# Optimization experiments

Hardware: AMD Instinct MI355X
Metric: run time of the kernel (lower is better)

Reference implementation:

```python
import jax, jax.numpy as jnp
import numpy as np
from jax import lax

GAIN = 2.0 ** (-0.5)
EPS = 1e-8


def _modconv(x, style_vec, s_w, s_b, weight):
    # x: [b, cin, h, w]; style_vec: [b, style_dim]
    # s_w: [cin, style_dim], s_b: [cin]; weight: [cout, cin, k, k]
    style_dim = s_w.shape[1]
    scale = GAIN * style_dim ** (-0.5)  # EqualizedLinear scale on input
    style = (style_vec * scale) @ s_w.T + s_b            # [b, cin]
    w = weight[None] * style[:, None, :, None, None]     # [b, cout, cin, k, k]
    demod = lax.rsqrt(jnp.sum(w * w, axis=(2, 3, 4)) + EPS)  # [b, cout]
    w = w * demod[:, :, None, None, None]

    def conv_one(xi, wi):
        # xi: [cin, h, w], wi: [cout, cin, k, k]
        return lax.conv_general_dilated(
            xi[None], wi, window_strides=(1, 1), padding='SAME',
            dimension_numbers=('NCHW', 'OIHW', 'NCHW'))[0]

    return jax.vmap(conv_one)(x, w)  # [b, cout, h, w]


def setup_inputs() -> dict:
    key = jax.random.key(0)
    ks = jax.random.split(key, 13)
    B, Cin, Cout, S, H, W = 16, 256, 256, 512, 64, 64
    f32 = jnp.float32
    return {
        'x': jax.random.normal(ks[0], (B, Cin, H, W), f32),
        'w1': jax.random.normal(ks[1], (B, S), f32),
        'w2': jax.random.normal(ks[2], (B, S), f32),
        'noise1': jax.random.normal(ks[3], (B, 1, H, W), f32),
        'noise2': jax.random.normal(ks[4], (B, 1, H, W), f32),
        's1_w': jax.random.normal(ks[5], (Cin, S), f32),
        's1_b': jnp.zeros((Cin,), f32),
        'conv1_w': jax.random.normal(ks[6], (Cout, Cin, 3, 3), f32),
        'nw1': 0.1 * jax.random.normal(ks[7], (Cout,), f32),
        's2_w': jax.random.normal(ks[8], (Cout, S), f32),
        's2_b': jnp.zeros((Cout,), f32),
        'conv2_w': jax.random.normal(ks[9], (Cout, Cout, 3, 3), f32),
        'nw2': 0.1 * jax.random.normal(ks[10], (Cout,), f32),
    }


def reference(x, w1, w2, noise1, noise2, s1_w, s1_b, conv1_w, nw1,
              s2_w, s2_b, conv2_w, nw2):
    h = _modconv(x, w1, s1_w, s1_b, conv1_w)
    h = h + nw1[None, :, None, None] * noise1
    h = jax.nn.leaky_relu(h, 0.2)
    h = _modconv(h, w2, s2_w, s2_b, conv2_w)
    h = h + nw2[None, :, None, None] * noise2
    return jax.nn.leaky_relu(h, 0.2)
```

## Files before the change

### kernel.cpp

```cpp
#include <hip/hip_runtime.h>
#include <cstdint>
#include <cstddef>

typedef _Float16 f16;
typedef _Float16 f16x8 __attribute__((ext_vector_type(8)));
typedef _Float16 f16x4 __attribute__((ext_vector_type(4)));
typedef float    f32x4 __attribute__((ext_vector_type(4)));

typedef const void __attribute__((address_space(1))) gconst_void;
typedef void __attribute__((address_space(3)))       lds_void;

#define LDS_IN_HALF_ELEMS (6*66*40)
#define LDS_IN_BYTES      (2*6*66*40*2)
#define WTILE_BYTES       8192
#define SMEM_TOTAL        (LDS_IN_BYTES + 2*WTILE_BYTES)
#define WF_BYTES          (16ULL*144*8192)

__device__ __forceinline__ int lin_idx(int half, int row, int col, int ci) {
    return ((half*6 + row)*66 + col)*40 + ci;
}

__device__ __forceinline__ void gll16(const char* g, char* l) {
    __builtin_amdgcn_global_load_lds((gconst_void*)g, (lds_void*)l, 16, 0, 0);
}

__global__ __launch_bounds__(256) void prep_kernel(
    const float* __restrict__ style_vec,
    const float* __restrict__ s_w,
    const float* __restrict__ s_b,
    const float* __restrict__ conv_w,
    f16* __restrict__ wf)
{
    const int b = blockIdx.x & 15;
    const int g = blockIdx.x >> 4;
    const int t = threadIdx.x;
    __shared__ float style[256];
    {
        const float4* sv = (const float4*)(style_vec + b*512);
        const float4* sw = (const float4*)(s_w + (size_t)t*512);
        float acc = 0.f;
        for (int i = 0; i < 128; ++i) {
            float4 a = sv[i], w = sw[i];
            acc += a.x*w.x + a.y*w.y + a.z*w.z + a.w*w.w;
        }
        style[t] = acc * 0.03125f + s_b[t];
    }
    __syncthreads();

    const int cout = g*32 + (t >> 3);
    const int sub  = t & 7;
    const int cin0 = sub * 32;
    const float* wrow = conv_w + (size_t)cout * 2304;

    float ss = 0.f;
    for (int ci = 0; ci < 32; ++ci) {
        float st = style[cin0 + ci];
        const float* wp = wrow + (cin0 + ci)*9;
        #pragma unroll
        for (int kk = 0; kk < 9; ++kk) { float v = wp[kk]*st; ss += v*v; }
    }
    ss += __shfl_xor(ss, 1);
    ss += __shfl_xor(ss, 2);
    ss += __shfl_xor(ss, 4);
    const float dem = 64.f / sqrtf(ss + 1e-8f);

    const int ch = cout >> 7;
    const int m  = (cout >> 4) & 7;
    const int lane_lo = cout & 15;
    const size_t bch_base = ((size_t)b*144 + ch) * 4096;

    for (int kg = 0; kg < 4; ++kg) {
        float stv[8];
        #pragma unroll
        for (int j = 0; j < 8; ++j) stv[j] = style[cin0 + kg*8 + j] * dem;
        for (int kk = 0; kk < 9; ++kk) {
            f16x8 hi;
            #pragma unroll
            for (int j = 0; j < 8; ++j)
                hi[j] = (f16)(wrow[(cin0 + kg*8 + j)*9 + kk] * stv[j]);
            size_t off = bch_base + (size_t)((kk*8 + sub)*2) * 4096
                       + (size_t)(m*64 + lane_lo + 16*kg) * 8;
            *(f16x8*)(wf + off) = hi;
        }
    }
}

template<int MODE>
__global__ __launch_bounds__(256, 2) void conv_kernel(
    const float*    __restrict__ in32,
    const uint32_t* __restrict__ in_pair,
    const f16*      __restrict__ wf,
    const float*    __restrict__ noise,
    const float*    __restrict__ nw,
    float*          __restrict__ out32,
    uint32_t*       __restrict__ out_pair)
{
    extern __shared__ __align__(16) char smem[];
    f16*  lds_in = (f16*)smem;
    char* wbuf   = smem + LDS_IN_BYTES;

    const int tid  = threadIdx.x;
    const int bid  = blockIdx.x;
    const int b    = bid & 15;
    const int y0   = ((bid >> 4) & 15) * 4;
    const int ch   = bid >> 8;
    const int lane = tid & 63;
    const int wn   = tid >> 6;
    const int lcol = lane & 15;
    const int kg   = lane >> 4;

    const char* wf_bch = (const char*)wf + ((size_t)b*144 + ch) * WTILE_BYTES;

    auto stage_w = [&](int ck_, int t_, int buf_) {
        const char* gsw = wf_bch + (size_t)((t_*8 + ck_)*2) * WTILE_BYTES;
        char* lsw = wbuf + buf_ * WTILE_BYTES;
        gll16(gsw + tid*16, lsw + tid*16);
        gll16(gsw + 4096 + tid*16, lsw + 4096 + tid*16);
    };

    stage_w(0, 0, 0);

    for (int e = tid; e < 2*6*2*40; e += 256) {
        int half = e / 480; int rem = e - half*480;
        int row = rem / 80; int rem2 = rem - row*80;
        int side = rem2 / 40; int ci = rem2 - side*40;
        lds_in[lin_idx(half, row, side ? 65 : 0, ci)] = (f16)0.f;
    }

    f32x4 acc[8][4];
    #pragma unroll
    for (int m = 0; m < 8; ++m)
        #pragma unroll
        for (int n = 0; n < 4; ++n)
            acc[m][n] = (f32x4){0.f, 0.f, 0.f, 0.f};

    const int y = y0 + wn;
    float nz[4];
    #pragma unroll
    for (int n = 0; n < 4; ++n) nz[n] = noise[b*4096 + y*64 + n*16 + lcol];

    #pragma unroll 1
    for (int ck = 0; ck < 8; ++ck) {
        __syncthreads();

        #pragma unroll 3
        for (int i = 0; i < 12; ++i) {
            int grp = i*256 + tid;
            int col, row, ci0;
            if (MODE == 0) { col = grp & 63; row = (grp >> 6) % 6; ci0 = (grp / 384) * 4; }
            else           { ci0 = (grp & 7) * 4; col = (grp >> 3) & 63; row = grp >> 9; }
            int gy = y0 - 1 + row;
            f16x4 hi4 = (f16x4){(f16)0.f,(f16)0.f,(f16)0.f,(f16)0.f};
            f16x4 lo4 = hi4;
            if (gy >= 0 && gy < 64) {
                if (MODE == 0) {
                    const float* p = in32 + ((size_t)(b*256 + ck*32 + ci0))*4096 + gy*64 + col;
                    #pragma unroll
                    for (int k = 0; k < 4; ++k) {
                        float xv = p[(size_t)k*4096] * 64.f;
                        f16 h = (f16)xv;
                        hi4[k] = h;
                        lo4[k] = (f16)(xv - (float)h);
                    }
                } else {
                    const f16x8 pr = *(const f16x8*)(in_pair +
                        ((size_t)((b*8 + ck)*64 + gy)*64 + col)*32 + ci0);
                    hi4 = __builtin_shufflevector(pr, pr, 0, 2, 4, 6);
                    lo4 = __builtin_shufflevector(pr, pr, 1, 3, 5, 7);
                }
            }
            *(f16x4*)(lds_in + lin_idx(0, row, col + 1, ci0)) = hi4;
            *(f16x4*)(lds_in + lin_idx(1, row, col + 1, ci0)) = lo4;
        }

        __syncthreads();

        #pragma unroll
        for (int t = 0; t < 9; ++t) {
            if (t) __syncthreads();
            if (t < 8)        stage_w(ck, t+1, (ck + t + 1) & 1);
            else if (ck < 7)  stage_w(ck+1, 0, (ck + 1) & 1);

            const int kh = t / 3, kw = t - kh*3;
            const f16* wcur = (const f16*)(wbuf + ((ck + t) & 1) * WTILE_BYTES);

            f16x8 bhi[4], blo[4];
            #pragma unroll
            for (int n = 0; n < 4; ++n) {
                int e = ((wn + kh)*66 + n*16 + lcol + kw)*40 + kg*8;
                bhi[n] = *(const f16x8*)(lds_in + e);
                blo[n] = *(const f16x8*)(lds_in + e + LDS_IN_HALF_ELEMS);
            }
            __builtin_amdgcn_s_setprio(1);
            #pragma unroll
            for (int m = 0; m < 8; ++m) {
                f16x8 a = *(const f16x8*)(wcur + m*512 + lane*8);
                #pragma unroll
                for (int n = 0; n < 4; ++n) {
                    acc[m][n] = __builtin_amdgcn_mfma_f32_16x16x32_f16(a, bhi[n], acc[m][n], 0, 0, 0);
                    acc[m][n] = __builtin_amdgcn_mfma_f32_16x16x32_f16(a, blo[n], acc[m][n], 0, 0, 0);
                }
            }
            __builtin_amdgcn_s_setprio(0);
        }
    }

    const float inv = 1.f / 4096.f;
    #pragma unroll
    for (int m = 0; m < 8; ++m) {
        const int coutb = ch*128 + m*16 + kg*4;
        float nwv[4];
        #pragma unroll
        for (int r = 0; r < 4; ++r) nwv[r] = nw[coutb + r];
        #pragma unroll
        for (int n = 0; n < 4; ++n) {
            const int col = n*16 + lcol;
            #pragma unroll
            for (int r = 0; r < 4; ++r) {
                float v = acc[m][n][r]*inv + nwv[r]*nz[n];
                v = fmaxf(v, 0.2f*v);
                const int cout = coutb + r;
                if (MODE == 0) {
                    float vs = v * 64.f;
                    f16 h = (f16)vs;
                    f16 l = (f16)(vs - (float)h);
                    uint32_t pk = (uint32_t)__builtin_bit_cast(uint16_t, h)
                                | ((uint32_t)__builtin_bit_cast(uint16_t, l) << 16);
                    size_t idx = (((size_t)(b*8 + (cout >> 5))*64 + y)*64 + col)*32 + (cout & 31);
                    out_pair[idx] = pk;
                } else {
                    out32[((size_t)(b*256 + cout))*4096 + y*64 + col] = v;
                }
            }
        }
    }
}

extern "C" void kernel_launch(void* const* d_in, const int* in_sizes, int n_in,
                              void* d_out, int out_size, void* d_ws, size_t ws_size,
                              hipStream_t stream) {
    (void)in_sizes; (void)n_in; (void)out_size; (void)ws_size;
    const float* x      = (const float*)d_in[0];
    const float* w1     = (const float*)d_in[1];
    const float* w2     = (const float*)d_in[2];
    const float* noise1 = (const float*)d_in[3];
    const float* noise2 = (const float*)d_in[4];
    const float* s1w    = (const float*)d_in[5];
    const float* s1b    = (const float*)d_in[6];
    const float* c1w    = (const float*)d_in[7];
    const float* nw1    = (const float*)d_in[8];
    const float* s2w    = (const float*)d_in[9];
    const float* s2b    = (const float*)d_in[10];
    const float* c2w    = (const float*)d_in[11];
    const float* nw2    = (const float*)d_in[12];
    float* out = (float*)d_out;

    f16*      wf    = (f16*)d_ws;
    uint32_t* hpair = (uint32_t*)((char*)d_ws + WF_BYTES);

    (void)hipFuncSetAttribute(reinterpret_cast<const void*>(&conv_kernel<0>),
                              hipFuncAttributeMaxDynamicSharedMemorySize, SMEM_TOTAL);
    (void)hipFuncSetAttribute(reinterpret_cast<const void*>(&conv_kernel<1>),
                              hipFuncAttributeMaxDynamicSharedMemorySize, SMEM_TOTAL);

    prep_kernel<<<128, 256, 0, stream>>>(w1, s1w, s1b, c1w, wf);
    conv_kernel<0><<<512, 256, SMEM_TOTAL, stream>>>(x, nullptr, wf, noise1, nw1, nullptr, hpair);
    prep_kernel<<<128, 256, 0, stream>>>(w2, s2w, s2b, c2w, wf);
    conv_kernel<1><<<512, 256, SMEM_TOTAL, stream>>>(nullptr, hpair, wf, noise2, nw2, out, nullptr);
}
```

Measured before the change: 535.1 us.

## Load weight fragments directly from global into registers instead of LDS staging

Removes the double-buffered global_load_lds staging of weight tiles and the per-tap __syncthreads, so each wave reads its A fragments straight from global memory (L2) into registers. This is meant to cut LDS traffic, shrink the LDS footprint and remove seven barriers per channel chunk. In exchange, every wave (four per block) loads the same weight tile separately from global memory, and there is no explicit prefetch, so load latency may be exposed right before the MFMA loop. Register pressure also rises from holding eight A fragments at once.

```diff
diff --git a/kernel.cpp b/kernel.cpp
--- a/kernel.cpp
+++ b/kernel.cpp
@@ -7,21 +7,13 @@
 typedef _Float16 f16x4 __attribute__((ext_vector_type(4)));
 typedef float    f32x4 __attribute__((ext_vector_type(4)));
 
-typedef const void __attribute__((address_space(1))) gconst_void;
-typedef void __attribute__((address_space(3)))       lds_void;
-
 #define LDS_IN_HALF_ELEMS (6*66*40)
 #define LDS_IN_BYTES      (2*6*66*40*2)
-#define WTILE_BYTES       8192
-#define SMEM_TOTAL        (LDS_IN_BYTES + 2*WTILE_BYTES)
+#define SMEM_TOTAL        LDS_IN_BYTES
 #define WF_BYTES          (16ULL*144*8192)
 
 __device__ __forceinline__ int lin_idx(int half, int row, int col, int ci) {
     return ((half*6 + row)*66 + col)*40 + ci;
-}
-
-__device__ __forceinline__ void gll16(const char* g, char* l) {
-    __builtin_amdgcn_global_load_lds((gconst_void*)g, (lds_void*)l, 16, 0, 0);
 }
 
 __global__ __launch_bounds__(256) void prep_kernel(
@@ -96,8 +88,7 @@
     uint32_t*       __restrict__ out_pair)
 {
     extern __shared__ __align__(16) char smem[];
-    f16*  lds_in = (f16*)smem;
-    char* wbuf   = smem + LDS_IN_BYTES;
+    f16* lds_in = (f16*)smem;
 
     const int tid  = threadIdx.x;
     const int bid  = blockIdx.x;
@@ -109,16 +100,7 @@
     const int lcol = lane & 15;
     const int kg   = lane >> 4;
 
-    const char* wf_bch = (const char*)wf + ((size_t)b*144 + ch) * WTILE_BYTES;
-
-    auto stage_w = [&](int ck_, int t_, int buf_) {
-        const char* gsw = wf_bch + (size_t)((t_*8 + ck_)*2) * WTILE_BYTES;
-        char* lsw = wbuf + buf_ * WTILE_BYTES;
-        gll16(gsw + tid*16, lsw + tid*16);
-        gll16(gsw + 4096 + tid*16, lsw + 4096 + tid*16);
-    };
-
-    stage_w(0, 0, 0);
+    const f16* wf_bch = wf + ((size_t)b*144 + ch) * 4096;
 
     for (int e = tid; e < 2*6*2*40; e += 256) {
         int half = e / 480; int rem = e - half*480;
@@ -177,12 +159,12 @@
 
         #pragma unroll
         for (int t = 0; t < 9; ++t) {
-            if (t) __syncthreads();
-            if (t < 8)        stage_w(ck, t+1, (ck + t + 1) & 1);
-            else if (ck < 7)  stage_w(ck+1, 0, (ck + 1) & 1);
-
             const int kh = t / 3, kw = t - kh*3;
-            const f16* wcur = (const f16*)(wbuf + ((ck + t) & 1) * WTILE_BYTES);
+
+            const f16* wt = wf_bch + (size_t)((t*8 + ck)*2) * 4096 + lane*8;
+            f16x8 a[8];
+            #pragma unroll
+            for (int m = 0; m < 8; ++m) a[m] = *(const f16x8*)(wt + m*512);
 
             f16x8 bhi[4], blo[4];
             #pragma unroll
@@ -191,14 +173,14 @@
                 bhi[n] = *(const f16x8*)(lds_in + e);
                 blo[n] = *(const f16x8*)(lds_in + e + LDS_IN_HALF_ELEMS);
             }
+
             __builtin_amdgcn_s_setprio(1);
             #pragma unroll
             for (int m = 0; m < 8; ++m) {
-                f16x8 a = *(const f16x8*)(wcur + m*512 + lane*8);
                 #pragma unroll
                 for (int n = 0; n < 4; ++n) {
-                    acc[m][n] = __builtin_amdgcn_mfma_f32_16x16x32_f16(a, bhi[n], acc[m][n], 0, 0, 0);
-                    acc[m][n] = __builtin_amdgcn_mfma_f32_16x16x32_f16(a, blo[n], acc[m][n], 0, 0, 0);
+                    acc[m][n] = __builtin_amdgcn_mfma_f32_16x16x32_f16(a[m], bhi[n], acc[m][n], 0, 0, 0);
+                    acc[m][n] = __builtin_amdgcn_mfma_f32_16x16x32_f16(a[m], blo[n], acc[m][n], 0, 0, 0);
                 }
             }
             __builtin_amdgcn_s_setprio(0);
```

Result: faster. 509.9 us (-4.7%).
